# Performance work log

Hardware: AMD Instinct MI355X
Metric: run time of the kernel (lower is better)

The kernel has to match this reference:

```python
import jax, jax.numpy as jnp
import numpy as np

N = 50000        # nodes
E = 800000       # edges
F_IN = 64
HID = [128, 256, 256]
G = 512          # graphs in batch
C = 6            # classes
EPS = 1e-5


def setup_inputs() -> dict:
    key = jax.random.key(0)
    ks = jax.random.split(key, 32)
    inp = {}
    inp['x'] = jax.random.normal(ks[0], (N, F_IN), dtype=jnp.float32)
    inp['edge_index'] = jax.random.randint(ks[1], (2, E), 0, N, dtype=jnp.int64)
    inp['batch'] = jnp.sort(jax.random.randint(ks[2], (N,), 0, G, dtype=jnp.int64))
    dims = [F_IN] + HID
    i = 3
    for l in range(3):
        d_in, d_out = dims[l], dims[l + 1]
        inp[f'W{l+1}'] = jax.random.normal(ks[i], (d_in, d_out), dtype=jnp.float32) * (1.0 / np.sqrt(d_in)); i += 1
        inp[f'b{l+1}'] = jnp.zeros((d_out,), dtype=jnp.float32)
        inp[f'g{l+1}'] = jnp.ones((d_out,), dtype=jnp.float32)
        inp[f'be{l+1}'] = jnp.zeros((d_out,), dtype=jnp.float32)
        inp[f'm{l+1}'] = jax.random.normal(ks[i], (d_out,), dtype=jnp.float32) * 0.1; i += 1
        inp[f'v{l+1}'] = jax.random.uniform(ks[i], (d_out,), dtype=jnp.float32, minval=0.5, maxval=1.5); i += 1
    mlp_dims = [(2 * HID[-1], 256), (256, 128), (128, C)]
    for l, (d_in, d_out) in enumerate(mlp_dims):
        inp[f'Wm{l+1}'] = jax.random.normal(ks[i], (d_in, d_out), dtype=jnp.float32) * (1.0 / np.sqrt(d_in)); i += 1
        inp[f'bm{l+1}'] = jnp.zeros((d_out,), dtype=jnp.float32)
    return inp


def _forward(x, edge_index, batch,
             W1, b1, g1, be1, m1, v1,
             W2, b2, g2, be2, m2, v2,
             W3, b3, g3, be3, m3, v3,
             Wm1, bm1, Wm2, bm2, Wm3, bm3):
    src, dst = edge_index[0], edge_index[1]
    loops = jnp.arange(N, dtype=src.dtype)
    src_sl = jnp.concatenate([src, loops])   # self-loops, as in PyG GCNConv
    dst_sl = jnp.concatenate([dst, loops])
    deg = jax.ops.segment_sum(jnp.ones_like(src_sl, dtype=x.dtype), dst_sl, num_segments=N)
    dis = jnp.where(deg > 0, jax.lax.rsqrt(deg), 0.0)
    norm = dis[src_sl] * dis[dst_sl]          # [E+N]

    def gcn(h, W, b):
        h = h @ W                              # transform first (PyG order)
        msg = h[src_sl] * norm[:, None]        # gather + scale
        return jax.ops.segment_sum(msg, dst_sl, num_segments=N) + b

    def bn_relu(h, g, be, m, v):
        return jax.nn.relu((h - m) * jax.lax.rsqrt(v + EPS) * g + be)

    h = bn_relu(gcn(x, W1, b1), g1, be1, m1, v1)
    h = bn_relu(gcn(h, W2, b2), g2, be2, m2, v2)
    h = bn_relu(gcn(h, W3, b3), g3, be3, m3, v3)

    counts = jax.ops.segment_sum(jnp.ones((N,), dtype=h.dtype), batch, num_segments=G)
    x_mean = jax.ops.segment_sum(h, batch, num_segments=G) / jnp.maximum(counts, 1.0)[:, None]
    x_max = jax.ops.segment_max(h, batch, num_segments=G)
    x_max = jnp.where(counts[:, None] > 0, x_max, 0.0)
    z = jnp.concatenate([x_mean, x_max], axis=1)   # [G, 512]

    z = jax.nn.gelu(z @ Wm1 + bm1, approximate=False)
    z = jax.nn.gelu(z @ Wm2 + bm2, approximate=False)
    return z @ Wm3 + bm3                            # [G, C]


def reference(x, edge_index, batch,
              W1, b1, g1, be1, m1, v1,
              W2, b2, g2, be2, m2, v2,
              W3, b3, g3, be3, m3, v3,
              Wm1, bm1, Wm2, bm2, Wm3, bm3):
    return _forward(x, edge_index, batch,
                    W1, b1, g1, be1, m1, v1,
                    W2, b2, g2, be2, m2, v2,
                    W3, b3, g3, be3, m3, v3,
                    Wm1, bm1, Wm2, bm2, Wm3, bm3)
```

## Files before the change

### kernel.cpp

```cpp
#include <hip/hip_runtime.h>
#include <hip/hip_bf16.h>
#include <hip/hip_fp16.h>

typedef __hip_bfloat16 bf16;
typedef unsigned short u16;
typedef short bfrag __attribute__((ext_vector_type(8)));
typedef float f32x4 __attribute__((ext_vector_type(4)));
typedef unsigned u32x2 __attribute__((ext_vector_type(2)));

#define NGRAPH 512
#define BN_EPS 1e-5f
#define NBUCK 64

__device__ __forceinline__ float b2f(bf16 x) { return __bfloat162float(x); }
__device__ __forceinline__ float bf_lo(unsigned u) { return __uint_as_float(u << 16); }
__device__ __forceinline__ float bf_hi(unsigned u) { return __uint_as_float(u & 0xffff0000u); }
__device__ __forceinline__ u16 f2u(float v) {
    bf16 t = __float2bfloat16(v);
    u16 r; __builtin_memcpy(&r, &t, 2); return r;
}

__device__ __forceinline__ float load_f(const void* p, int i, int isbf16) {
    if (isbf16) {
        unsigned short u = ((const unsigned short*)p)[i];
        return __uint_as_float(((unsigned int)u) << 16);
    }
    return ((const float*)p)[i];
}

__device__ __forceinline__ void repack_sec(const void* W, u16* out, int Kd, int Nd,
                                           int t, int isbf) {
    if (t >= Kd * Nd) return;
    int j = t & 7;
    int lane = (t >> 3) & 63;
    int tile = t >> 9;
    int NT = Nd / 16;
    int nt = tile % NT, kt = tile / NT;
    int k = kt * 32 + (lane >> 4) * 8 + j;
    int nn = nt * 16 + (lane & 15);
    out[t] = f2u(load_f(W, k * Nd + nn, isbf));
}

__device__ __forceinline__ void fold_one(const void* b, const void* g, const void* be,
                                         const void* m, const void* v,
                                         float* S, float* T, int f, int isbf) {
    float bb = load_f(b, f, isbf), gg = load_f(g, f, isbf);
    float bee = load_f(be, f, isbf), mm = load_f(m, f, isbf);
    float vv = load_f(v, f, isbf);
    float s = gg * rsqrtf(vv + BN_EPS);
    S[f] = s;
    T[f] = (bb - mm) * s + bee;
}

__global__ void prep_all(
    const void* __restrict__ x,
    const void* W1, const void* W2, const void* W3,
    const void* b1, const void* g1, const void* be1, const void* m1, const void* v1,
    const void* b2, const void* g2, const void* be2, const void* m2, const void* v2,
    const void* b3, const void* g3, const void* be3, const void* m3, const void* v3,
    u16* __restrict__ xs, u16* W1r, u16* W2r, u16* W3r,
    float* S1, float* T1, float* S2, float* T2, float* S3, float* T3,
    int* __restrict__ deg, int* __restrict__ total, int* __restrict__ bcnt,
    int* __restrict__ claim, float* __restrict__ psum, float* __restrict__ pmax,
    int* __restrict__ pcnt,
    int n, int npad, int* __restrict__ flag) {
    __shared__ int lflag;
    if (threadIdx.x < 64) {
        unsigned short u = ((const unsigned short*)x)[2 * threadIdx.x];
        float f = __uint_as_float(((unsigned int)u) << 16);
        int crazy = (!(fabsf(f) <= 1024.0f)) ? 1 : 0;
        unsigned long long m = __ballot(crazy);
        if (threadIdx.x == 0) lflag = (m == 0ULL) ? 1 : 0;
    }
    __syncthreads();
    const int isbf = lflag;
    const int bid = blockIdx.x;
    const int tid = threadIdx.x;
    if (bid == 0 && tid == 0) *flag = isbf;

    const int nb_cvt = (n * 64 + 255) / 256;
    if (bid < nb_cvt) {
        int i = bid * 256 + tid;
        if (i < n * 64) {
            int node = i >> 6, f = i & 63;
            xs[((size_t)(f >> 5) * npad + node) * 32 + (f & 31)] = f2u(load_f(x, i, isbf));
        }
        return;
    }
    int b2_ = bid - nb_cvt;
    if (b2_ < 32)  { repack_sec(W1, W1r, 64, 128, b2_ * 256 + tid, isbf); return; }
    b2_ -= 32;
    if (b2_ < 128) { repack_sec(W2, W2r, 128, 256, b2_ * 256 + tid, isbf); return; }
    b2_ -= 128;
    if (b2_ < 256) { repack_sec(W3, W3r, 256, 256, b2_ * 256 + tid, isbf); return; }
    b2_ -= 256;
    if (b2_ < 3) {
        int t = b2_ * 256 + tid;
        if (t < 128) fold_one(b1, g1, be1, m1, v1, S1, T1, t, isbf);
        else if (t < 384) fold_one(b2, g2, be2, m2, v2, S2, T2, t - 128, isbf);
        else if (t < 640) fold_one(b3, g3, be3, m3, v3, S3, T3, t - 384, isbf);
        return;
    }
    b2_ -= 3;
    {
        int i = b2_ * 256 + tid;
        if (i < n) deg[i] = 0;
        if (i < NGRAPH * 256) { psum[i] = 0.f; pmax[i] = 0.f; }
        if (i < NGRAPH) pcnt[i] = 0;
        if (i < NBUCK) { bcnt[i] = 0; claim[i] = 0; }
        if (i == 0) *total = 0;
    }
}

__global__ void count_deg_i(const int* __restrict__ dst, int* __restrict__ deg, int e) {
    int i = blockIdx.x * blockDim.x + threadIdx.x;
    if (i < e) atomicAdd(&deg[dst[i]], 1);
}

__global__ void reserve_rows(const int* __restrict__ deg, int* __restrict__ row_start,
                             int* __restrict__ cursor, float* __restrict__ dis,
                             unsigned* __restrict__ csrw,
                             int* __restrict__ total, int* __restrict__ bcnt, int n) {
    __shared__ int lh[NBUCK];
    int tid = threadIdx.x;
    if (tid < NBUCK) lh[tid] = 0;
    __syncthreads();
    int i = blockIdx.x * blockDim.x + tid;
    if (i < n) {
        int d = deg[i];
        int dpad = (d + 7) & ~7;
        int s = atomicAdd(total, dpad);
        row_start[i] = s;
        cursor[i] = s;
        dis[i] = rsqrtf((float)(d + 1));
        atomicAdd(&lh[min(d, NBUCK - 1)], 1);
        unsigned val = (unsigned)(i & 0xffff);
        for (int k = d; k < dpad; k++) csrw[s + k] = val;
    }
    __syncthreads();
    if (tid < NBUCK) {
        int c = lh[tid];
        if (c) atomicAdd(&bcnt[tid], c);
    }
}

__global__ void scatter_all(const int* __restrict__ src, const int* __restrict__ dst,
                            const float* __restrict__ dis, int* __restrict__ cursor,
                            unsigned* __restrict__ csrw,
                            const int* __restrict__ deg, const int* __restrict__ rowst,
                            const int* __restrict__ bcnt, int* __restrict__ claim,
                            uint4* __restrict__ ninfo, int e, int n, int nbE) {
    int bid = blockIdx.x;
    int tid = threadIdx.x;
    if (bid < nbE) {
        int i = bid * 256 + tid;
        if (i >= e) return;
        int s = src[i], dt = dst[i];
        int pos = atomicAdd(&cursor[dt], 1);
        float nw = dis[s] * dis[dt];
        unsigned short h = __half_as_ushort(__float2half(nw));
        csrw[pos] = (unsigned)(s & 0xffff) | ((unsigned)h << 16);
        return;
    }
    __shared__ int lh[NBUCK];
    __shared__ int lbase[NBUCK];
    __shared__ int lpre[NBUCK];
    if (tid < NBUCK) lh[tid] = 0;
    if (tid == 0) {
        int acc = 0;
        for (int k = 0; k < NBUCK; k++) { lpre[k] = acc; acc += bcnt[k]; }
    }
    __syncthreads();
    int i = (bid - nbE) * 256 + tid;
    int b = 0, lr = 0;
    if (i < n) {
        b = min(deg[i], NBUCK - 1);
        lr = atomicAdd(&lh[b], 1);
    }
    __syncthreads();
    if (tid < NBUCK) {
        int c = lh[tid];
        lbase[tid] = c ? (lpre[tid] + atomicAdd(&claim[tid], c)) : 0;
    }
    __syncthreads();
    if (i < n) ninfo[lbase[b] + lr] = make_uint4(i, rowst[i], deg[i], 0);
}

template <int NSLICE>
__global__ __launch_bounds__(256) void csr_agg_s5(
    const uint4* __restrict__ ninfo, const unsigned* __restrict__ csrw,
    const u16* __restrict__ hs, u16* __restrict__ AG, int n, int npad) {
    constexpr int F = NSLICE * 32;
    int slice = blockIdx.x % NSLICE;
    int nb = blockIdx.x / NSLICE;
    int lane = threadIdx.x & 63;
    int wv = threadIdx.x >> 6;
    int sub = lane >> 3, ls = lane & 7;
    int oidx = nb * 32 + wv * 8 + sub;
    if (oidx >= n) return;
    uint4 nf = ninfo[oidx];
    int node = (int)nf.x;
    int start = (int)nf.y;
    int d = (int)nf.z;
    int dpad = (d + 7) & ~7;
    float dd = 1.0f / (float)(d + 1);
    const u16* __restrict__ base = hs + (size_t)slice * npad * 32;

    float a0, a1, a2, a3;
    {
        uint2 u = *(const uint2*)(base + (size_t)node * 32 + ls * 4);
        a0 = bf_lo(u.x) * dd; a1 = bf_hi(u.x) * dd;
        a2 = bf_lo(u.y) * dd; a3 = bf_hi(u.y) * dd;
    }

    const unsigned* __restrict__ ep = csrw + start;
    unsigned mc[8];
    if (dpad) {
#pragma unroll
        for (int j = 0; j < 8; j++) mc[j] = ep[j];
    }
    for (int k = 0; k < dpad; k += 8) {
        unsigned mn[8];
        if (k + 8 < dpad) {
#pragma unroll
            for (int j = 0; j < 8; j++) mn[j] = ep[k + 8 + j];
        }
        float w[8];
        uint2 q[8];
#pragma unroll
        for (int j = 0; j < 8; j++) {
            int s = (int)(mc[j] & 0xffffu);
            w[j] = __half2float(__ushort_as_half((unsigned short)(mc[j] >> 16)));
            q[j] = *(const uint2*)(base + (size_t)s * 32 + ls * 4);
        }
#pragma unroll
        for (int j = 0; j < 8; j++) {
            a0 += w[j] * bf_lo(q[j].x); a1 += w[j] * bf_hi(q[j].x);
            a2 += w[j] * bf_lo(q[j].y); a3 += w[j] * bf_hi(q[j].y);
        }
#pragma unroll
        for (int j = 0; j < 8; j++) mc[j] = mn[j];
    }
    u32x2 o;
    o.x = (unsigned)f2u(a0) | ((unsigned)f2u(a1) << 16);
    o.y = (unsigned)f2u(a2) | ((unsigned)f2u(a3) << 16);
    __builtin_nontemporal_store(o, (u32x2*)(AG + (size_t)node * F + slice * 32 + ls * 4));
}

template <int K, int N, int NSUB, int NSLICE_OUT>
__global__ __launch_bounds__(256) void mfma_gemm_dg(
    const u16* __restrict__ A, const u16* __restrict__ Wrep,
    const float* __restrict__ S, const float* __restrict__ T,
    u16* __restrict__ C, int M, int npad, int ntiles) {
    constexpr int NT = N / 16;
    constexpr int KT = K / 32;
    constexpr int NSPLIT = NT / NSUB;
    int bid = blockIdx.x;
    int g = bid >> 3;
    int ns = g % NSPLIT;
    int mt = (bid & 7) + 8 * (g / NSPLIT);
    if (mt >= ntiles) return;
    const int tid = threadIdx.x;
    const int lane = tid & 63;
    const int wv = tid >> 6;
    const int mrow = lane & 15;
    const int kb = lane >> 4;

    bfrag breg[KT * NSUB];
#pragma unroll
    for (int kt = 0; kt < KT; kt++)
#pragma unroll
        for (int j = 0; j < NSUB; j++)
            breg[kt * NSUB + j] = *(const bfrag*)(Wrep +
                ((size_t)(kt * NT + ns * NSUB + j) * 64 + lane) * 8);

    const u16* __restrict__ arow = A + (size_t)(mt * 64 + wv * 16 + mrow) * K + kb * 8;
    bfrag areg[KT];
#pragma unroll
    for (int kt = 0; kt < KT; kt++)
        areg[kt] = *(const bfrag*)(arow + kt * 32);

    f32x4 acc[NSUB];
#pragma unroll
    for (int j = 0; j < NSUB; j++) acc[j] = (f32x4){0.f, 0.f, 0.f, 0.f};
#pragma unroll
    for (int kt = 0; kt < KT; kt++)
#pragma unroll
        for (int j = 0; j < NSUB; j++)
            acc[j] = __builtin_amdgcn_mfma_f32_16x16x32_bf16(areg[kt], breg[kt * NSUB + j], acc[j], 0, 0, 0);

    const int m0 = mt * 64;
#pragma unroll
    for (int j = 0; j < NSUB; j++) {
        int f = (ns * NSUB + j) * 16 + mrow;
        float s = S[f];
        float t = T[f];
#pragma unroll
        for (int r = 0; r < 4; r++) {
            int row = m0 + wv * 16 + kb * 4 + r;
            if (row < M) {
                u16 val = f2u(fmaxf(acc[j][r] * s + t, 0.0f));
                if (NSLICE_OUT > 0)
                    C[((size_t)(f >> 5) * npad + row) * 32 + (f & 31)] = val;
                else
                    C[(size_t)row * N + f] = val;
            }
        }
    }
}

#define POOL_NC 64
__global__ __launch_bounds__(256) void pool_seg(
    const u16* __restrict__ h, const int* __restrict__ batch,
    float* __restrict__ psum, float* __restrict__ pmax,
    int* __restrict__ pcnt, int n) {
    int wid = (int)(((size_t)blockIdx.x * blockDim.x + threadIdx.x) >> 6);
    int lane = threadIdx.x & 63;
    int n0 = wid * POOL_NC;
    if (n0 >= n) return;
    int n1 = min(n0 + POOL_NC, n);

    float sum[4] = {0.f, 0.f, 0.f, 0.f};
    float mx[4] = {0.f, 0.f, 0.f, 0.f};
    int cnt = 0;
    int gcur = batch[n0];

    uint2 u_next = *(const uint2*)(h + (size_t)n0 * 256 + lane * 4);
    int g_next = gcur;

    for (int node = n0; node < n1; node++) {
        uint2 u = u_next;
        int g = g_next;
        if (node + 1 < n1) {
            u_next = *(const uint2*)(h + (size_t)(node + 1) * 256 + lane * 4);
            g_next = batch[node + 1];
        }
        if (g != gcur) {
#pragma unroll
            for (int c = 0; c < 4; c++) {
                atomicAdd(&psum[gcur * 256 + lane * 4 + c], sum[c]);
                atomicMax((int*)&pmax[gcur * 256 + lane * 4 + c], __float_as_int(mx[c]));
                sum[c] = 0.f; mx[c] = 0.f;
            }
            if (lane == 0) atomicAdd(&pcnt[gcur], cnt);
            cnt = 0;
            gcur = g;
        }
        float v0 = bf_lo(u.x), v1 = bf_hi(u.x), v2 = bf_lo(u.y), v3 = bf_hi(u.y);
        sum[0] += v0; sum[1] += v1; sum[2] += v2; sum[3] += v3;
        mx[0] = fmaxf(mx[0], v0); mx[1] = fmaxf(mx[1], v1);
        mx[2] = fmaxf(mx[2], v2); mx[3] = fmaxf(mx[3], v3);
        cnt++;
    }
#pragma unroll
    for (int c = 0; c < 4; c++) {
        atomicAdd(&psum[gcur * 256 + lane * 4 + c], sum[c]);
        atomicMax((int*)&pmax[gcur * 256 + lane * 4 + c], __float_as_int(mx[c]));
    }
    if (lane == 0) atomicAdd(&pcnt[gcur], cnt);
}

__global__ __launch_bounds__(256) void mlp_fused(
    const float* __restrict__ psum, const float* __restrict__ pmax,
    const int* __restrict__ pcnt,
    const void* __restrict__ Wm1, const void* __restrict__ bm1,
    const void* __restrict__ Wm2, const void* __restrict__ bm2,
    const void* __restrict__ Wm3, const void* __restrict__ bm3,
    void* __restrict__ out, const int* __restrict__ flag) {
    __shared__ float a[512];
    __shared__ float h1[256];
    __shared__ float h2[128];
    int row = blockIdx.x;
    int tid = threadIdx.x;
    int isbf = *flag;
    float invc = 1.0f / (float)max(pcnt[row], 1);
    a[tid] = psum[row * 256 + tid] * invc;
    a[256 + tid] = pmax[row * 256 + tid];
    __syncthreads();
    {
        float acc = load_f(bm1, tid, isbf);
        if (isbf) {
            const bf16* w = (const bf16*)Wm1;
            for (int k = 0; k < 512; k++) acc += a[k] * b2f(w[k * 256 + tid]);
        } else {
            const float* w = (const float*)Wm1;
            for (int k = 0; k < 512; k++) acc += a[k] * w[k * 256 + tid];
        }
        h1[tid] = 0.5f * acc * (1.0f + erff(acc * 0.70710678118654752f));
    }
    __syncthreads();
    if (tid < 128) {
        float acc = load_f(bm2, tid, isbf);
        if (isbf) {
            const bf16* w = (const bf16*)Wm2;
            for (int k = 0; k < 256; k++) acc += h1[k] * b2f(w[k * 128 + tid]);
        } else {
            const float* w = (const float*)Wm2;
            for (int k = 0; k < 256; k++) acc += h1[k] * w[k * 128 + tid];
        }
        h2[tid] = 0.5f * acc * (1.0f + erff(acc * 0.70710678118654752f));
    }
    __syncthreads();
    if (tid < 6) {
        float acc = load_f(bm3, tid, isbf);
        if (isbf) {
            const bf16* w = (const bf16*)Wm3;
            for (int k = 0; k < 128; k++) acc += h2[k] * b2f(w[k * 6 + tid]);
        } else {
            const float* w = (const float*)Wm3;
            for (int k = 0; k < 128; k++) acc += h2[k] * w[k * 6 + tid];
        }
        if (isbf) ((bf16*)out)[row * 6 + tid] = __float2bfloat16(acc);
        else      ((float*)out)[row * 6 + tid] = acc;
    }
}

extern "C" void kernel_launch(void* const* d_in, const int* in_sizes, int n_in,
                              void* d_out, int out_size, void* d_ws, size_t ws_size,
                              hipStream_t stream) {
    const void* x     = d_in[0];
    const int*  ei    = (const int*)d_in[1];
    const int*  batch = (const int*)d_in[2];
    const void *W1 = d_in[3],  *b1 = d_in[4],  *g1 = d_in[5],  *be1 = d_in[6],  *m1 = d_in[7],  *v1 = d_in[8];
    const void *W2 = d_in[9],  *b2 = d_in[10], *g2 = d_in[11], *be2 = d_in[12], *m2 = d_in[13], *v2 = d_in[14];
    const void *W3 = d_in[15], *b3 = d_in[16], *g3 = d_in[17], *be3 = d_in[18], *m3 = d_in[19], *v3 = d_in[20];
    const void *Wm1 = d_in[21], *bm1 = d_in[22];
    const void *Wm2 = d_in[23], *bm2 = d_in[24];
    const void *Wm3 = d_in[25], *bm3 = d_in[26];

    const int n = in_sizes[0] / 64;
    const int E = in_sizes[1] / 2;
    const int* src = ei;
    const int* dst = ei + E;
    const int npad = (n + 63 + 64) & ~63;
    const int ntiles = (n + 63) / 64;
    const int ntp8 = (ntiles + 7) & ~7;

    size_t off = 0;
    auto carve = [&](size_t bytes) {
        void* p = (char*)d_ws + off;
        off += (bytes + 255) & ~(size_t)255;
        return p;
    };
    int*      flag  = (int*)carve(4);
    int*      total = (int*)carve(4);
    int*      bcnt  = (int*)carve(NBUCK * 4);
    int*      claim = (int*)carve(NBUCK * 4);
    float*    dis   = (float*)carve((size_t)n * 4);
    int*      deg_i = (int*)carve((size_t)n * 4);
    int*      rowst = (int*)carve((size_t)n * 4);
    int*      curs  = (int*)carve((size_t)n * 4);
    uint4*    ninfo = (uint4*)carve((size_t)n * 16);
    unsigned* csrw  = (unsigned*)carve(((size_t)E + 8 * (size_t)n) * 4);
    u16*      xs    = (u16*)carve((size_t)npad * 64 * 2);
    u16*      Hs    = (u16*)carve((size_t)npad * 256 * 2);
    u16*      AG    = (u16*)carve((size_t)npad * 256 * 2);
    u16*      H     = (u16*)carve((size_t)npad * 256 * 2);
    u16*      W1r   = (u16*)carve((size_t)64 * 128 * 2);
    u16*      W2r   = (u16*)carve((size_t)128 * 256 * 2);
    u16*      W3r   = (u16*)carve((size_t)256 * 256 * 2);
    float* S1 = (float*)carve(128 * 4); float* T1 = (float*)carve(128 * 4);
    float* S2 = (float*)carve(256 * 4); float* T2 = (float*)carve(256 * 4);
    float* S3 = (float*)carve(256 * 4); float* T3 = (float*)carve(256 * 4);
    float* psum = (float*)carve((size_t)NGRAPH * 256 * 4);
    float* pmax = (float*)carve((size_t)NGRAPH * 256 * 4);
    int*   pcnt = (int*)carve((size_t)NGRAPH * 4);
    (void)ws_size; (void)n_in;

    const int BT = 256;

    const int nb_cvt = (n * 64 + 255) / 256;
    const int nb_init = (NGRAPH * 256 + 255) / 256;
    prep_all<<<nb_cvt + 32 + 128 + 256 + 3 + nb_init, BT, 0, stream>>>(
        x, W1, W2, W3,
        b1, g1, be1, m1, v1, b2, g2, be2, m2, v2, b3, g3, be3, m3, v3,
        xs, W1r, W2r, W3r, S1, T1, S2, T2, S3, T3,
        deg_i, total, bcnt, claim, psum, pmax, pcnt, n, npad, flag);

    count_deg_i<<<(E + BT - 1) / BT, BT, 0, stream>>>(dst, deg_i, E);
    reserve_rows<<<(n + BT - 1) / BT, BT, 0, stream>>>(deg_i, rowst, curs, dis, csrw, total, bcnt, n);
    const int nbE = (E + BT - 1) / BT;
    const int nbN = (n + BT - 1) / BT;
    scatter_all<<<nbE + nbN, BT, 0, stream>>>(src, dst, dis, curs, csrw,
                                              deg_i, rowst, bcnt, claim, ninfo, E, n, nbE);

    const int nb32 = (n + 31) / 32;

    csr_agg_s5<2><<<2 * nb32, 256, 0, stream>>>(ninfo, csrw, xs, AG, n, npad);
    mfma_gemm_dg<64, 128, 4, 4><<<2 * ntp8, 256, 0, stream>>>(AG, W1r, S1, T1, Hs, n, npad, ntiles);

    csr_agg_s5<4><<<4 * nb32, 256, 0, stream>>>(ninfo, csrw, Hs, AG, n, npad);
    mfma_gemm_dg<128, 256, 4, 8><<<4 * ntp8, 256, 0, stream>>>(AG, W2r, S2, T2, Hs, n, npad, ntiles);

    csr_agg_s5<8><<<8 * nb32, 256, 0, stream>>>(ninfo, csrw, Hs, AG, n, npad);
    mfma_gemm_dg<256, 256, 2, 0><<<8 * ntp8, 256, 0, stream>>>(AG, W3r, S3, T3, H, n, npad, ntiles);

    const int pool_waves = (n + POOL_NC - 1) / POOL_NC;
    pool_seg<<<(pool_waves * 64 + BT - 1) / BT, BT, 0, stream>>>(H, batch, psum, pmax, pcnt, n);
    mlp_fused<<<NGRAPH, 256, 0, stream>>>(psum, pmax, pcnt, Wm1, bm1, Wm2, bm2, Wm3, bm3, d_out, flag);
}
```

Measured before the change: 436.1 us.

## Lay out CSR rows in degree-bucket order so neighboring workers read contiguous rows

Replaces the global atomic row reservation with a bucketed layout. Nodes are histogrammed by padded degree (in units of 8), and each row's start offset is computed from bucket prefix sums, so rows assigned to adjacent ninfo entries sit next to each other in csrw. The aggregation kernels should then read memory more sequentially, and the single-counter atomic contention on row reservation goes away. The cost is one extra kernel launch, since the node and edge scatter are now split, plus an overflow path for very high-degree nodes that allocates from the end of the buffer.

```diff
diff --git a/kernel.cpp b/kernel.cpp
--- a/kernel.cpp
+++ b/kernel.cpp
@@ -60,7 +60,7 @@
     const void* b3, const void* g3, const void* be3, const void* m3, const void* v3,
     u16* __restrict__ xs, u16* W1r, u16* W2r, u16* W3r,
     float* S1, float* T1, float* S2, float* T2, float* S3, float* T3,
-    int* __restrict__ deg, int* __restrict__ total, int* __restrict__ bcnt,
+    int* __restrict__ deg, int* __restrict__ ovf, int* __restrict__ bcnt,
     int* __restrict__ claim, float* __restrict__ psum, float* __restrict__ pmax,
     int* __restrict__ pcnt,
     int n, int npad, int* __restrict__ flag) {
@@ -108,7 +108,7 @@
         if (i < NGRAPH * 256) { psum[i] = 0.f; pmax[i] = 0.f; }
         if (i < NGRAPH) pcnt[i] = 0;
         if (i < NBUCK) { bcnt[i] = 0; claim[i] = 0; }
-        if (i == 0) *total = 0;
+        if (i == 0) *ovf = 0;
     }
 }
 
@@ -117,10 +117,8 @@
     if (i < e) atomicAdd(&deg[dst[i]], 1);
 }
 
-__global__ void reserve_rows(const int* __restrict__ deg, int* __restrict__ row_start,
-                             int* __restrict__ cursor, float* __restrict__ dis,
-                             unsigned* __restrict__ csrw,
-                             int* __restrict__ total, int* __restrict__ bcnt, int n) {
+__global__ void hist_rows(const int* __restrict__ deg, float* __restrict__ dis,
+                          int* __restrict__ bcnt, int n) {
     __shared__ int lh[NBUCK];
     int tid = threadIdx.x;
     if (tid < NBUCK) lh[tid] = 0;
@@ -128,14 +126,8 @@
     int i = blockIdx.x * blockDim.x + tid;
     if (i < n) {
         int d = deg[i];
-        int dpad = (d + 7) & ~7;
-        int s = atomicAdd(total, dpad);
-        row_start[i] = s;
-        cursor[i] = s;
         dis[i] = rsqrtf((float)(d + 1));
-        atomicAdd(&lh[min(d, NBUCK - 1)], 1);
-        unsigned val = (unsigned)(i & 0xffff);
-        for (int k = d; k < dpad; k++) csrw[s + k] = val;
+        atomicAdd(&lh[min((d + 7) >> 3, NBUCK - 1)], 1);
     }
     __syncthreads();
     if (tid < NBUCK) {
@@ -144,46 +136,63 @@
     }
 }
 
-__global__ void scatter_all(const int* __restrict__ src, const int* __restrict__ dst,
-                            const float* __restrict__ dis, int* __restrict__ cursor,
-                            unsigned* __restrict__ csrw,
-                            const int* __restrict__ deg, const int* __restrict__ rowst,
-                            const int* __restrict__ bcnt, int* __restrict__ claim,
-                            uint4* __restrict__ ninfo, int e, int n, int nbE) {
-    int bid = blockIdx.x;
-    int tid = threadIdx.x;
-    if (bid < nbE) {
-        int i = bid * 256 + tid;
-        if (i >= e) return;
-        int s = src[i], dt = dst[i];
-        int pos = atomicAdd(&cursor[dt], 1);
-        float nw = dis[s] * dis[dt];
-        unsigned short h = __half_as_ushort(__float2half(nw));
-        csrw[pos] = (unsigned)(s & 0xffff) | ((unsigned)h << 16);
-        return;
-    }
+__global__ void node_scatter(const int* __restrict__ deg, const int* __restrict__ bcnt,
+                             int* __restrict__ claim, int* __restrict__ ovf,
+                             int* __restrict__ cursor, unsigned* __restrict__ csrw,
+                             uint4* __restrict__ ninfo, int n, int cap) {
     __shared__ int lh[NBUCK];
     __shared__ int lbase[NBUCK];
-    __shared__ int lpre[NBUCK];
+    __shared__ int cpre[NBUCK];
+    __shared__ int wpre[NBUCK];
+    int tid = threadIdx.x;
     if (tid < NBUCK) lh[tid] = 0;
-    if (tid == 0) {
-        int acc = 0;
-        for (int k = 0; k < NBUCK; k++) { lpre[k] = acc; acc += bcnt[k]; }
-    }
-    __syncthreads();
-    int i = (bid - nbE) * 256 + tid;
-    int b = 0, lr = 0;
+    if (tid == 64) {
+        int ca = 0, wa = 0;
+        for (int k = 0; k < NBUCK; k++) {
+            cpre[k] = ca; wpre[k] = wa;
+            ca += bcnt[k]; wa += bcnt[k] * 8 * k;
+        }
+    }
+    __syncthreads();
+    int i = blockIdx.x * blockDim.x + tid;
+    int b = 0, lr = 0, d = 0;
     if (i < n) {
-        b = min(deg[i], NBUCK - 1);
+        d = deg[i];
+        b = min((d + 7) >> 3, NBUCK - 1);
         lr = atomicAdd(&lh[b], 1);
     }
     __syncthreads();
     if (tid < NBUCK) {
         int c = lh[tid];
-        lbase[tid] = c ? (lpre[tid] + atomicAdd(&claim[tid], c)) : 0;
-    }
-    __syncthreads();
-    if (i < n) ninfo[lbase[b] + lr] = make_uint4(i, rowst[i], deg[i], 0);
+        lbase[tid] = c ? atomicAdd(&claim[tid], c) : 0;
+    }
+    __syncthreads();
+    if (i >= n) return;
+    int rank = lbase[b] + lr;
+    int pos = cpre[b] + rank;
+    int dpad = (d + 7) & ~7;
+    int start;
+    if (b < NBUCK - 1) {
+        start = wpre[b] + rank * 8 * b;
+    } else {
+        start = cap - atomicAdd(ovf, dpad) - dpad;
+    }
+    cursor[i] = start;
+    unsigned val = (unsigned)(i & 0xffff);
+    for (int k = d; k < dpad; k++) csrw[start + k] = val;
+    ninfo[pos] = make_uint4(i, start, d, 0);
+}
+
+__global__ void edge_scatter(const int* __restrict__ src, const int* __restrict__ dst,
+                             const float* __restrict__ dis, int* __restrict__ cursor,
+                             unsigned* __restrict__ csrw, int e) {
+    int i = blockIdx.x * blockDim.x + threadIdx.x;
+    if (i >= e) return;
+    int s = src[i], dt = dst[i];
+    int pos = atomicAdd(&cursor[dt], 1);
+    float nw = dis[s] * dis[dt];
+    unsigned short h = __half_as_ushort(__float2half(nw));
+    csrw[pos] = (unsigned)(s & 0xffff) | ((unsigned)h << 16);
 }
 
 template <int NSLICE>
@@ -435,6 +444,7 @@
     const int npad = (n + 63 + 64) & ~63;
     const int ntiles = (n + 63) / 64;
     const int ntp8 = (ntiles + 7) & ~7;
+    const int cap = E + 8 * n;
 
     size_t off = 0;
     auto carve = [&](size_t bytes) {
@@ -443,15 +453,14 @@
         return p;
     };
     int*      flag  = (int*)carve(4);
-    int*      total = (int*)carve(4);
+    int*      ovf   = (int*)carve(4);
     int*      bcnt  = (int*)carve(NBUCK * 4);
     int*      claim = (int*)carve(NBUCK * 4);
     float*    dis   = (float*)carve((size_t)n * 4);
     int*      deg_i = (int*)carve((size_t)n * 4);
-    int*      rowst = (int*)carve((size_t)n * 4);
     int*      curs  = (int*)carve((size_t)n * 4);
     uint4*    ninfo = (uint4*)carve((size_t)n * 16);
-    unsigned* csrw  = (unsigned*)carve(((size_t)E + 8 * (size_t)n) * 4);
+    unsigned* csrw  = (unsigned*)carve((size_t)cap * 4);
     u16*      xs    = (u16*)carve((size_t)npad * 64 * 2);
     u16*      Hs    = (u16*)carve((size_t)npad * 256 * 2);
     u16*      AG    = (u16*)carve((size_t)npad * 256 * 2);
@@ -475,14 +484,13 @@
         x, W1, W2, W3,
         b1, g1, be1, m1, v1, b2, g2, be2, m2, v2, b3, g3, be3, m3, v3,
         xs, W1r, W2r, W3r, S1, T1, S2, T2, S3, T3,
-        deg_i, total, bcnt, claim, psum, pmax, pcnt, n, npad, flag);
+        deg_i, ovf, bcnt, claim, psum, pmax, pcnt, n, npad, flag);
 
     count_deg_i<<<(E + BT - 1) / BT, BT, 0, stream>>>(dst, deg_i, E);
-    reserve_rows<<<(n + BT - 1) / BT, BT, 0, stream>>>(deg_i, rowst, curs, dis, csrw, total, bcnt, n);
-    const int nbE = (E + BT - 1) / BT;
-    const int nbN = (n + BT - 1) / BT;
-    scatter_all<<<nbE + nbN, BT, 0, stream>>>(src, dst, dis, curs, csrw,
-                                              deg_i, rowst, bcnt, claim, ninfo, E, n, nbE);
+    hist_rows<<<(n + BT - 1) / BT, BT, 0, stream>>>(deg_i, dis, bcnt, n);
+    node_scatter<<<(n + BT - 1) / BT, BT, 0, stream>>>(deg_i, bcnt, claim, ovf,
+                                                       curs, csrw, ninfo, n, cap);
+    edge_scatter<<<(E + BT - 1) / BT, BT, 0, stream>>>(src, dst, dis, curs, csrw, E);
 
     const int nb32 = (n + 31) / 32;
 
```

Result: faster. 417.4 us (-4.3%).
